# Kernel optimization log

Measured on AMD Instinct MI355X. Metric: run time of the kernel, lower is better.

Reference implementation:

```python
import jax, jax.numpy as jnp
import numpy as np

T_STEPS = 30
HIDDEN = 16
INPUT_DIM = 32
OUTPUT_DIM = 1
BATCH = 262144


def setup_inputs() -> dict:
    key = jax.random.key(0)
    ks = jax.random.split(key, 8)
    u = lambda k, shape: jax.random.uniform(k, shape, jnp.float32, -0.25, 0.25)
    return {
        "x": jax.random.normal(ks[0], (BATCH, INPUT_DIM), jnp.float32),
        "T": T_STEPS,
        "W_ih": u(ks[1], (HIDDEN, INPUT_DIM)),
        "W_hh": u(ks[2], (HIDDEN, HIDDEN)),
        "b_ih": u(ks[3], (HIDDEN,)),
        "b_hh": u(ks[4], (HIDDEN,)),
        "W_fc": jax.random.normal(ks[5], (OUTPUT_DIM, HIDDEN), jnp.float32) * 0.25,
        "b_fc": jax.random.normal(ks[6], (OUTPUT_DIM,), jnp.float32) * 0.25,
    }


def reference(x, T, W_ih, W_hh, b_ih, b_hh, W_fc, b_fc):
    # Input is the same at every timestep (x repeated T times), so the
    # input projection is computed once and reused across the scan.
    xproj = x @ W_ih.T + b_ih + b_hh  # [B, H]
    h0 = jnp.zeros((x.shape[0], W_hh.shape[0]), dtype=x.dtype)

    def step(h, _):
        h = jnp.tanh(xproj + h @ W_hh.T)  # Elman: tanh(Wx+b_ih + Uh+b_hh)
        return h, h

    _, hs = jax.lax.scan(step, h0, None, length=T)  # [T, B, H]
    hs = jnp.transpose(hs, (1, 0, 2))               # [B, T, H] (batch_first)
    return hs @ W_fc.T + b_fc                       # [B, T, output_dim]
```

## Files before the change

kernel.cpp:

```cpp
#include <hip/hip_runtime.h>


#define T_STEPS 30
#define BLOCK   128
#define SCALE   2.8853900817779268f

typedef _Float16 v4h __attribute__((ext_vector_type(4)));
typedef __fp16   v2fp __attribute__((ext_vector_type(2)));
typedef float    v4f __attribute__((ext_vector_type(4)));
typedef float    v2f __attribute__((ext_vector_type(2)));

struct h4 { v2fp lo, hi; };

static __device__ __forceinline__ v4h pack4(float a, float b, float c, float d) {
    h4 p;
    p.lo = __builtin_amdgcn_cvt_pkrtz(a, b);
    p.hi = __builtin_amdgcn_cvt_pkrtz(c, d);
    return __builtin_bit_cast(v4h, p);
}

__global__ __launch_bounds__(BLOCK, 8) void rnn_mfma(
    const float* __restrict__ x,
    const float* __restrict__ W_ih,
    const float* __restrict__ W_hh,
    const float* __restrict__ b_ih,
    const float* __restrict__ b_hh,
    const float* __restrict__ W_fc,
    const float* __restrict__ b_fc,
    float* __restrict__ out)
{
    __shared__ float tmp[32 * T_STEPS];

    const int tid  = threadIdx.x;
    const int w    = tid >> 6;
    const int lane = tid & 63;
    const int r    = lane & 15;
    const int q    = lane >> 4;
    const int j0   = 4 * q;

    const size_t row = (size_t)blockIdx.x * 32 + (size_t)w * 16 + r;

    v4f xpv;
    {
        const float4 x0 = *(const float4*)(x + row * 32 + 4 * q);
        const float4 x1 = *(const float4*)(x + row * 32 + 16 + 4 * q);
        float4 w0 = *(const float4*)(W_ih + r * 32 + 4 * q);
        float4 w1 = *(const float4*)(W_ih + r * 32 + 16 + 4 * q);
        w0.x *= SCALE; w0.y *= SCALE; w0.z *= SCALE; w0.w *= SCALE;
        w1.x *= SCALE; w1.y *= SCALE; w1.z *= SCALE; w1.w *= SCALE;

        v4h xh0 = pack4(x0.x, x0.y, x0.z, x0.w);
        v4h xh1 = pack4(x1.x, x1.y, x1.z, x1.w);
        v4h wh0 = pack4(w0.x, w0.y, w0.z, w0.w);
        v4h wh1 = pack4(w1.x, w1.y, w1.z, w1.w);
        v4h xl0 = pack4(x0.x - (float)xh0[0], x0.y - (float)xh0[1],
                        x0.z - (float)xh0[2], x0.w - (float)xh0[3]);
        v4h xl1 = pack4(x1.x - (float)xh1[0], x1.y - (float)xh1[1],
                        x1.z - (float)xh1[2], x1.w - (float)xh1[3]);
        v4h wl0 = pack4(w0.x - (float)wh0[0], w0.y - (float)wh0[1],
                        w0.z - (float)wh0[2], w0.w - (float)wh0[3]);
        v4h wl1 = pack4(w1.x - (float)wh1[0], w1.y - (float)wh1[1],
                        w1.z - (float)wh1[2], w1.w - (float)wh1[3]);

        const float4 bi = *(const float4*)(b_ih + j0);
        const float4 bh = *(const float4*)(b_hh + j0);
        v4f c = {SCALE * (bi.x + bh.x), SCALE * (bi.y + bh.y),
                 SCALE * (bi.z + bh.z), SCALE * (bi.w + bh.w)};

        xpv = __builtin_amdgcn_mfma_f32_16x16x16f16(wh0, xh0, c,   0, 0, 0);
        xpv = __builtin_amdgcn_mfma_f32_16x16x16f16(wh1, xh1, xpv, 0, 0, 0);
        xpv = __builtin_amdgcn_mfma_f32_16x16x16f16(wh0, xl0, xpv, 0, 0, 0);
        xpv = __builtin_amdgcn_mfma_f32_16x16x16f16(wh1, xl1, xpv, 0, 0, 0);
        xpv = __builtin_amdgcn_mfma_f32_16x16x16f16(wl0, xh0, xpv, 0, 0, 0);
        xpv = __builtin_amdgcn_mfma_f32_16x16x16f16(wl1, xh1, xpv, 0, 0, 0);
    }

    v4h whh;
    {
        float4 wr = *(const float4*)(W_hh + r * 16 + 4 * q);
        whh[0] = (_Float16)(wr.x * SCALE);
        whh[1] = (_Float16)(wr.y * SCALE);
        whh[2] = (_Float16)(wr.z * SCALE);
        whh[3] = (_Float16)(wr.w * SCALE);
    }

    v4h afc;
#pragma unroll
    for (int i = 0; i < 4; ++i) {
        float wv = W_fc[4 * q + i];
        _Float16 hi = (_Float16)wv;
        _Float16 lo = (_Float16)(wv - (float)hi);
        afc[i] = (r == 0) ? hi : ((r == 1) ? lo : (_Float16)0.0f);
    }
    const float bfc = b_fc[0];
    const v4f zfc = {(q == 0) ? bfc : 0.0f, 0.0f, 0.0f, 0.0f};

    v4h s = {(_Float16)0.0f, (_Float16)0.0f, (_Float16)0.0f, (_Float16)0.0f};

    float* myout = &tmp[(w * 16 + r) * T_STEPS];

    const v2f one2  = {1.0f, 1.0f};
    const v2f mtwo2 = {-2.0f, -2.0f};

    v4f fe, fo;

#pragma unroll
    for (int t = 0; t < T_STEPS; ++t) {
        v4f acc = __builtin_amdgcn_mfma_f32_16x16x16f16(whh, s, xpv, 0, 0, 0);

        v2f eU = {__builtin_amdgcn_exp2f(acc[0]), __builtin_amdgcn_exp2f(acc[2])};
        v2f eV = {__builtin_amdgcn_exp2f(acc[1]), __builtin_amdgcn_exp2f(acc[3])};
        v2f dU = eU + one2;
        v2f dV = eV + one2;
        v2f M  = dU * dV;
        float rr  = __builtin_amdgcn_rcpf(M.x * M.y);
        float r01 = rr * M.y;
        float r23 = rr * M.x;
        v2f Wsw  = {r01, r23};
        v2f invU = Wsw * dV;
        v2f invV = Wsw * dU;
        v2f hU = mtwo2 * invU + one2;
        v2f hV = mtwo2 * invV + one2;

        s = pack4(hU.x, hV.x, hU.y, hV.y);

        if ((t & 1) == 0) {
            if (t >= 2 && lane < 16) {
                float2 g;
                g.x = fe[0] + fe[1];
                g.y = fo[0] + fo[1];
                *(float2*)(myout + (t - 2)) = g;
            }
            fe = __builtin_amdgcn_mfma_f32_16x16x16f16(afc, s, zfc, 0, 0, 0);
        } else {
            fo = __builtin_amdgcn_mfma_f32_16x16x16f16(afc, s, zfc, 0, 0, 0);
        }
    }
    if (lane < 16) {
        float2 g;
        g.x = fe[0] + fe[1];
        g.y = fo[0] + fo[1];
        *(float2*)(myout + (T_STEPS - 2)) = g;
    }

    __syncthreads();

    float* oblk = out + (size_t)blockIdx.x * (32 * T_STEPS);
    for (int idx = tid; idx < 32 * T_STEPS; idx += BLOCK)
        oblk[idx] = tmp[idx];
}

extern "C" void kernel_launch(void* const* d_in, const int* in_sizes, int n_in,
                              void* d_out, int out_size, void* d_ws, size_t ws_size,
                              hipStream_t stream) {
    const float* x    = (const float*)d_in[0];
    const float* W_ih = (const float*)d_in[2];
    const float* W_hh = (const float*)d_in[3];
    const float* b_ih = (const float*)d_in[4];
    const float* b_hh = (const float*)d_in[5];
    const float* W_fc = (const float*)d_in[6];
    const float* b_fc = (const float*)d_in[7];
    float* out = (float*)d_out;

    const int B = in_sizes[0] / 32;
    const int grid = B / 32;

    rnn_mfma<<<grid, BLOCK, 0, stream>>>(x, W_ih, W_hh, b_ih, b_hh, W_fc, b_fc, out);
}
```

Measured before the change: 115.2 us.

## Process two independent 16-row recurrence chains per wavefront to hide MFMA latency

Each wavefront now handles two 16-row batch tiles. Their RNN recurrences are interleaved so each tile's MFMA and tanh latency is hidden behind the other's work. The W_ih split-precision weights and bias are computed once and shared by both tiles, and the grid is halved. This costs more registers and doubles the shared-memory staging buffer, which could lower occupancy, and there are fewer blocks to spread across the CUs.

```diff
diff --git a/kernel.cpp b/kernel.cpp
--- a/kernel.cpp
+++ b/kernel.cpp
@@ -29,7 +29,7 @@
     const float* __restrict__ b_fc,
     float* __restrict__ out)
 {
-    __shared__ float tmp[32 * T_STEPS];
+    __shared__ float tmp[64 * T_STEPS];
 
     const int tid  = threadIdx.x;
     const int w    = tid >> 6;
@@ -38,41 +38,48 @@
     const int q    = lane >> 4;
     const int j0   = 4 * q;
 
-    const size_t row = (size_t)blockIdx.x * 32 + (size_t)w * 16 + r;
+    const size_t rowA = (size_t)blockIdx.x * 64 + (size_t)w * 32 + r;
+    const size_t rowB = rowA + 16;
 
-    v4f xpv;
+    v4h wh0, wh1, wl0, wl1;
+    v4f cbias;
     {
-        const float4 x0 = *(const float4*)(x + row * 32 + 4 * q);
-        const float4 x1 = *(const float4*)(x + row * 32 + 16 + 4 * q);
         float4 w0 = *(const float4*)(W_ih + r * 32 + 4 * q);
         float4 w1 = *(const float4*)(W_ih + r * 32 + 16 + 4 * q);
         w0.x *= SCALE; w0.y *= SCALE; w0.z *= SCALE; w0.w *= SCALE;
         w1.x *= SCALE; w1.y *= SCALE; w1.z *= SCALE; w1.w *= SCALE;
+        wh0 = pack4(w0.x, w0.y, w0.z, w0.w);
+        wh1 = pack4(w1.x, w1.y, w1.z, w1.w);
+        wl0 = pack4(w0.x - (float)wh0[0], w0.y - (float)wh0[1],
+                    w0.z - (float)wh0[2], w0.w - (float)wh0[3]);
+        wl1 = pack4(w1.x - (float)wh1[0], w1.y - (float)wh1[1],
+                    w1.z - (float)wh1[2], w1.w - (float)wh1[3]);
+        const float4 bi = *(const float4*)(b_ih + j0);
+        const float4 bh = *(const float4*)(b_hh + j0);
+        cbias = (v4f){SCALE * (bi.x + bh.x), SCALE * (bi.y + bh.y),
+                      SCALE * (bi.z + bh.z), SCALE * (bi.w + bh.w)};
+    }
 
+    v4f xpvA, xpvB;
+#pragma unroll
+    for (int cc = 0; cc < 2; ++cc) {
+        const size_t row = cc ? rowB : rowA;
+        const float4 x0 = *(const float4*)(x + row * 32 + 4 * q);
+        const float4 x1 = *(const float4*)(x + row * 32 + 16 + 4 * q);
         v4h xh0 = pack4(x0.x, x0.y, x0.z, x0.w);
         v4h xh1 = pack4(x1.x, x1.y, x1.z, x1.w);
-        v4h wh0 = pack4(w0.x, w0.y, w0.z, w0.w);
-        v4h wh1 = pack4(w1.x, w1.y, w1.z, w1.w);
         v4h xl0 = pack4(x0.x - (float)xh0[0], x0.y - (float)xh0[1],
                         x0.z - (float)xh0[2], x0.w - (float)xh0[3]);
         v4h xl1 = pack4(x1.x - (float)xh1[0], x1.y - (float)xh1[1],
                         x1.z - (float)xh1[2], x1.w - (float)xh1[3]);
-        v4h wl0 = pack4(w0.x - (float)wh0[0], w0.y - (float)wh0[1],
-                        w0.z - (float)wh0[2], w0.w - (float)wh0[3]);
-        v4h wl1 = pack4(w1.x - (float)wh1[0], w1.y - (float)wh1[1],
-                        w1.z - (float)wh1[2], w1.w - (float)wh1[3]);
-
-        const float4 bi = *(const float4*)(b_ih + j0);
-        const float4 bh = *(const float4*)(b_hh + j0);
-        v4f c = {SCALE * (bi.x + bh.x), SCALE * (bi.y + bh.y),
-                 SCALE * (bi.z + bh.z), SCALE * (bi.w + bh.w)};
-
-        xpv = __builtin_amdgcn_mfma_f32_16x16x16f16(wh0, xh0, c,   0, 0, 0);
-        xpv = __builtin_amdgcn_mfma_f32_16x16x16f16(wh1, xh1, xpv, 0, 0, 0);
-        xpv = __builtin_amdgcn_mfma_f32_16x16x16f16(wh0, xl0, xpv, 0, 0, 0);
-        xpv = __builtin_amdgcn_mfma_f32_16x16x16f16(wh1, xl1, xpv, 0, 0, 0);
-        xpv = __builtin_amdgcn_mfma_f32_16x16x16f16(wl0, xh0, xpv, 0, 0, 0);
-        xpv = __builtin_amdgcn_mfma_f32_16x16x16f16(wl1, xh1, xpv, 0, 0, 0);
+        v4f xp;
+        xp = __builtin_amdgcn_mfma_f32_16x16x16f16(wh0, xh0, cbias, 0, 0, 0);
+        xp = __builtin_amdgcn_mfma_f32_16x16x16f16(wh1, xh1, xp,    0, 0, 0);
+        xp = __builtin_amdgcn_mfma_f32_16x16x16f16(wh0, xl0, xp,    0, 0, 0);
+        xp = __builtin_amdgcn_mfma_f32_16x16x16f16(wh1, xl1, xp,    0, 0, 0);
+        xp = __builtin_amdgcn_mfma_f32_16x16x16f16(wl0, xh0, xp,    0, 0, 0);
+        xp = __builtin_amdgcn_mfma_f32_16x16x16f16(wl1, xh1, xp,    0, 0, 0);
+        if (cc) xpvB = xp; else xpvA = xp;
     }
 
     v4h whh;
@@ -95,58 +102,68 @@
     const float bfc = b_fc[0];
     const v4f zfc = {(q == 0) ? bfc : 0.0f, 0.0f, 0.0f, 0.0f};
 
-    v4h s = {(_Float16)0.0f, (_Float16)0.0f, (_Float16)0.0f, (_Float16)0.0f};
+    v4h sA = {(_Float16)0.0f, (_Float16)0.0f, (_Float16)0.0f, (_Float16)0.0f};
+    v4h sB = sA;
 
-    float* myout = &tmp[(w * 16 + r) * T_STEPS];
+    float* myoutA = &tmp[(w * 32 + r) * T_STEPS];
+    float* myoutB = &tmp[(w * 32 + 16 + r) * T_STEPS];
 
     const v2f one2  = {1.0f, 1.0f};
     const v2f mtwo2 = {-2.0f, -2.0f};
 
-    v4f fe, fo;
+    v4f feA, foA, feB, foB;
 
 #pragma unroll
     for (int t = 0; t < T_STEPS; ++t) {
-        v4f acc = __builtin_amdgcn_mfma_f32_16x16x16f16(whh, s, xpv, 0, 0, 0);
+        v4f accA = __builtin_amdgcn_mfma_f32_16x16x16f16(whh, sA, xpvA, 0, 0, 0);
+        v4f accB = __builtin_amdgcn_mfma_f32_16x16x16f16(whh, sB, xpvB, 0, 0, 0);
 
-        v2f eU = {__builtin_amdgcn_exp2f(acc[0]), __builtin_amdgcn_exp2f(acc[2])};
-        v2f eV = {__builtin_amdgcn_exp2f(acc[1]), __builtin_amdgcn_exp2f(acc[3])};
-        v2f dU = eU + one2;
-        v2f dV = eV + one2;
-        v2f M  = dU * dV;
-        float rr  = __builtin_amdgcn_rcpf(M.x * M.y);
-        float r01 = rr * M.y;
-        float r23 = rr * M.x;
-        v2f Wsw  = {r01, r23};
-        v2f invU = Wsw * dV;
-        v2f invV = Wsw * dU;
-        v2f hU = mtwo2 * invU + one2;
-        v2f hV = mtwo2 * invV + one2;
+        v2f eUA = {__builtin_amdgcn_exp2f(accA[0]), __builtin_amdgcn_exp2f(accA[2])};
+        v2f eVA = {__builtin_amdgcn_exp2f(accA[1]), __builtin_amdgcn_exp2f(accA[3])};
+        v2f eUB = {__builtin_amdgcn_exp2f(accB[0]), __builtin_amdgcn_exp2f(accB[2])};
+        v2f eVB = {__builtin_amdgcn_exp2f(accB[1]), __builtin_amdgcn_exp2f(accB[3])};
 
-        s = pack4(hU.x, hV.x, hU.y, hV.y);
+        v2f dUA = eUA + one2, dVA = eVA + one2;
+        v2f dUB = eUB + one2, dVB = eVB + one2;
+        v2f MA = dUA * dVA;
+        v2f MB = dUB * dVB;
+        float rrA = __builtin_amdgcn_rcpf(MA.x * MA.y);
+        float rrB = __builtin_amdgcn_rcpf(MB.x * MB.y);
+        v2f WswA = {rrA * MA.y, rrA * MA.x};
+        v2f WswB = {rrB * MB.y, rrB * MB.x};
+        v2f invUA = WswA * dVA, invVA = WswA * dUA;
+        v2f invUB = WswB * dVB, invVB = WswB * dUB;
+        v2f hUA = mtwo2 * invUA + one2, hVA = mtwo2 * invVA + one2;
+        v2f hUB = mtwo2 * invUB + one2, hVB = mtwo2 * invVB + one2;
+
+        sA = pack4(hUA.x, hVA.x, hUA.y, hVA.y);
+        sB = pack4(hUB.x, hVB.x, hUB.y, hVB.y);
 
         if ((t & 1) == 0) {
             if (t >= 2 && lane < 16) {
-                float2 g;
-                g.x = fe[0] + fe[1];
-                g.y = fo[0] + fo[1];
-                *(float2*)(myout + (t - 2)) = g;
+                float2 gA = {feA[0] + feA[1], foA[0] + foA[1]};
+                float2 gB = {feB[0] + feB[1], foB[0] + foB[1]};
+                *(float2*)(myoutA + (t - 2)) = gA;
+                *(float2*)(myoutB + (t - 2)) = gB;
             }
-            fe = __builtin_amdgcn_mfma_f32_16x16x16f16(afc, s, zfc, 0, 0, 0);
+            feA = __builtin_amdgcn_mfma_f32_16x16x16f16(afc, sA, zfc, 0, 0, 0);
+            feB = __builtin_amdgcn_mfma_f32_16x16x16f16(afc, sB, zfc, 0, 0, 0);
         } else {
-            fo = __builtin_amdgcn_mfma_f32_16x16x16f16(afc, s, zfc, 0, 0, 0);
+            foA = __builtin_amdgcn_mfma_f32_16x16x16f16(afc, sA, zfc, 0, 0, 0);
+            foB = __builtin_amdgcn_mfma_f32_16x16x16f16(afc, sB, zfc, 0, 0, 0);
         }
     }
     if (lane < 16) {
-        float2 g;
-        g.x = fe[0] + fe[1];
-        g.y = fo[0] + fo[1];
-        *(float2*)(myout + (T_STEPS - 2)) = g;
+        float2 gA = {feA[0] + feA[1], foA[0] + foA[1]};
+        float2 gB = {feB[0] + feB[1], foB[0] + foB[1]};
+        *(float2*)(myoutA + (T_STEPS - 2)) = gA;
+        *(float2*)(myoutB + (T_STEPS - 2)) = gB;
     }
 
     __syncthreads();
 
-    float* oblk = out + (size_t)blockIdx.x * (32 * T_STEPS);
-    for (int idx = tid; idx < 32 * T_STEPS; idx += BLOCK)
+    float* oblk = out + (size_t)blockIdx.x * (64 * T_STEPS);
+    for (int idx = tid; idx < 64 * T_STEPS; idx += BLOCK)
         oblk[idx] = tmp[idx];
 }
 
@@ -163,7 +180,7 @@
     float* out = (float*)d_out;
 
     const int B = in_sizes[0] / 32;
-    const int grid = B / 32;
+    const int grid = B / 64;
 
     rnn_mfma<<<grid, BLOCK, 0, stream>>>(x, W_ih, W_hh, b_ih, b_hh, W_fc, b_fc, out);
 }
```

New measurement: 116.4 us. No clear change (+1.0%).
